# Optimization experiments

Hardware: AMD Instinct MI355X
Metric: run time of the kernel (lower is better)

The kernel has to match this reference:

```python
import jax, jax.numpy as jnp
import numpy as np

N_NODES = 15000
N_EDGES = 60000
NODE_VOCAB = 118 + 20000
EDGE_VOCAB = 4 + 50
NODE_INDIM = 64
EDGE_INDIM = 32
H = 32          # node_hidden_feats
EH = 64         # edge_hidden_feats
NUM_STEPS = 3   # num_step_message_passing
N_BOND_TYPES = 4  # edge ids < 4 are chemical bonds -> edge_func1, else knowledge relations -> edge_func2


def setup_inputs() -> dict:
    key = jax.random.key(0)
    ks = jax.random.split(key, 20)
    s = 0.05  # param scale for numerical stability
    return {
        "node_ids": jax.random.randint(ks[0], (N_NODES,), 0, NODE_VOCAB),
        "edge_ids": jax.random.randint(ks[1], (N_EDGES,), 0, EDGE_VOCAB),
        "src": jax.random.randint(ks[2], (N_EDGES,), 0, N_NODES),
        "dst": jax.random.randint(ks[3], (N_EDGES,), 0, N_NODES),
        "node_table": jax.random.normal(ks[4], (NODE_VOCAB, NODE_INDIM), jnp.float32),
        "edge_table": jax.random.normal(ks[5], (EDGE_VOCAB, EDGE_INDIM), jnp.float32),
        "proj_W": jax.random.normal(ks[6], (H, NODE_INDIM), jnp.float32) * s,
        "proj_b": jnp.zeros((H,), jnp.float32),
        "attn_w": jax.random.normal(ks[7], (2 * H,), jnp.float32) * s,
        "e1_W1": jax.random.normal(ks[8], (EH, EDGE_INDIM), jnp.float32) * s,
        "e1_b1": jnp.zeros((EH,), jnp.float32),
        "e1_W2": jax.random.normal(ks[9], (H * H, EH), jnp.float32) * s,
        "e1_b2": jnp.zeros((H * H,), jnp.float32),
        "e2_W1": jax.random.normal(ks[10], (EH, EDGE_INDIM), jnp.float32) * s,
        "e2_b1": jnp.zeros((EH,), jnp.float32),
        "e2_W2": jax.random.normal(ks[11], (H * H, EH), jnp.float32) * s,
        "e2_b2": jnp.zeros((H * H,), jnp.float32),
        "gru_Wih": jax.random.normal(ks[12], (3 * H, H), jnp.float32) * s,
        "gru_Whh": jax.random.normal(ks[13], (3 * H, H), jnp.float32) * s,
        "gru_bih": jnp.zeros((3 * H,), jnp.float32),
        "gru_bhh": jnp.zeros((3 * H,), jnp.float32),
    }


def _edge_softmax(logits, dst, num_nodes):
    # softmax over incoming edges of each destination node
    m = jax.ops.segment_max(logits, dst, num_segments=num_nodes)
    ex = jnp.exp(logits - m[dst])
    s = jax.ops.segment_sum(ex, dst, num_segments=num_nodes)
    return ex / s[dst]


def reference(node_ids, edge_ids, src, dst, node_table, edge_table, proj_W, proj_b,
              attn_w, e1_W1, e1_b1, e1_W2, e1_b2, e2_W1, e2_b1, e2_W2, e2_b2,
              gru_Wih, gru_Whh, gru_bih, gru_bhh):
    # --- embedding lookups ---
    nf = node_table[node_ids]                      # [N, node_indim]
    ef = edge_table[edge_ids]                      # [E, edge_indim]
    # --- project node feats: Linear + ReLU ---
    h = jax.nn.relu(nf @ proj_W.T + proj_b)        # [N, H]

    # --- per-edge weight matrices from the two edge MLPs (edge feats are
    # constant across message-passing steps, so compute once) ---
    def edge_mlp(W1, b1, W2, b2):
        z = jax.nn.relu(ef @ W1.T + b1)            # [E, EH]
        return (z @ W2.T + b2).reshape(-1, H, H)   # [E, H, H]

    W_e1 = edge_mlp(e1_W1, e1_b1, e1_W2, e1_b2)
    W_e2 = edge_mlp(e2_W1, e2_b1, e2_W2, e2_b2)
    is_bond = (edge_ids < N_BOND_TYPES)[:, None, None]
    W_edge = jnp.where(is_bond, W_e1, W_e2)        # [E, H, H]

    hidden = h                                     # GRU hidden state (seq of len 1 -> GRUCell)
    for _ in range(NUM_STEPS):
        # attention logits on edges: leaky_relu(attn_fc([h_src || h_dst]))
        a = jax.nn.leaky_relu(
            h[src] @ attn_w[:H] + h[dst] @ attn_w[H:])     # [E]
        alpha = _edge_softmax(a, dst, N_NODES)             # [E]
        # edge-conditioned message: (h_src @ W_e) weighted by attention
        msg = jnp.einsum('ei,eio->eo', h[src], W_edge) * alpha[:, None]  # [E, H]
        agg = jax.ops.segment_sum(msg, dst, num_segments=N_NODES)       # [N, H]
        m = jax.nn.relu(agg)
        # single GRU step (torch nn.GRU, 1 layer, seq_len 1)
        gi = m @ gru_Wih.T + gru_bih               # [N, 3H]
        gh = hidden @ gru_Whh.T + gru_bhh          # [N, 3H]
        ir, iz, inn = jnp.split(gi, 3, axis=1)
        hr, hz, hn = jnp.split(gh, 3, axis=1)
        r = jax.nn.sigmoid(ir + hr)
        z = jax.nn.sigmoid(iz + hz)
        n = jnp.tanh(inn + r * hn)
        hidden = (1.0 - z) * n + z * hidden
        h = hidden
    return h
```

## Files before the change

### kernel.cpp

```cpp
#include <hip/hip_runtime.h>
#include <math.h>

#define N_NODES   15000
#define N_EDGES   60000
#define EVOCAB    54
#define NODE_INDIM 64
#define EDGE_INDIM 32
#define H  32
#define EH 64
#define N_BOND 4

#define NPB   8
#define NBLK  (N_NODES / NPB)
#define CAPN  48

#define TASK_VOCAB (EVOCAB * 1024)
#define TASK_PROJ  (N_NODES * H)
#define TASK_EDGE_BASE (TASK_VOCAB + TASK_PROJ)
#define TA_TOTAL   (TASK_EDGE_BASE + N_EDGES)

#define WT_OFF   0
#define H0_OFF   221184
#define H1_OFF   2141184
#define W4_OFF   4061184
#define W2_OFF   4077568
#define LS0_OFF  4085760
#define BS0_OFF  4145760
#define LS1_OFF  4205760
#define BS1_OFF  4265760
#define CNT_OFF  4325760
#define EPK_OFF  4385760
#define W2T1_OFF 7265760
#define W2T2_OFF 7527904
#define PT_OFF   7790048

__global__ __launch_bounds__(256)
void pre_kernel(const float* __restrict__ e1_W2, const float* __restrict__ e2_W2,
                const float* __restrict__ proj_W,
                const float* __restrict__ gWih, const float* __restrict__ gWhh,
                float* __restrict__ W2T1, float* __restrict__ W2T2,
                float* __restrict__ PT,
                float4* __restrict__ Wpk4, float2* __restrict__ Wpk2,
                int* __restrict__ cnt)
{
    int b = blockIdx.x, tid = threadIdx.x;
    if (b < 32) {
        __shared__ float st[64][65];
        const float* in = (b < 16) ? e1_W2 : e2_W2;
        float* out      = (b < 16) ? W2T1  : W2T2;
        int f0 = (b & 15) * 64;
        #pragma unroll
        for (int it = 0; it < 16; ++it) {
            int idx = it * 256 + tid;
            int r = idx >> 6, c = idx & 63;
            st[r][c] = in[(f0 + r) * 64 + c];
        }
        __syncthreads();
        #pragma unroll
        for (int it = 0; it < 16; ++it) {
            int idx = it * 256 + tid;
            int k = idx >> 6, f = idx & 63;
            out[k * 1024 + f0 + f] = st[f][k];
        }
    } else if (b == 32) {
        __shared__ float sp2[64][33];
        #pragma unroll
        for (int it = 0; it < 8; ++it) {
            int idx = it * 256 + tid;
            int o = idx >> 6, j = idx & 63;
            sp2[j][o] = proj_W[idx];
        }
        __syncthreads();
        #pragma unroll
        for (int it = 0; it < 8; ++it) {
            int idx = it * 256 + tid;
            int j = idx >> 5, o = idx & 31;
            PT[idx] = sp2[j][o];
        }
    } else if (b <= 36) {
        int q = (b - 33) * 256 + tid;
        int j = q >> 5, o = q & 31;
        Wpk4[q] = make_float4(gWih[o * 32 + j], gWih[(32 + o) * 32 + j],
                              gWih[(64 + o) * 32 + j], gWhh[o * 32 + j]);
        Wpk2[q] = make_float2(gWhh[(32 + o) * 32 + j], gWhh[(64 + o) * 32 + j]);
    } else {
        int idx = (b - 37) * 256 + tid;
        if (idx < N_NODES) cnt[idx] = 0;
    }
}

__global__ __launch_bounds__(256)
void setup_kernel(const int* __restrict__ node_ids, const int* __restrict__ src,
                  const int* __restrict__ dst, const int* __restrict__ eid,
                  const float* __restrict__ node_table, const float* __restrict__ edge_table,
                  const float* __restrict__ PT, const float* __restrict__ proj_b,
                  const float* __restrict__ attn_w,
                  const float* __restrict__ e1_W1, const float* __restrict__ e1_b1,
                  const float* __restrict__ e1_b2,
                  const float* __restrict__ e2_W1, const float* __restrict__ e2_b1,
                  const float* __restrict__ e2_b2,
                  const float* __restrict__ W2T1, const float* __restrict__ W2T2,
                  float* __restrict__ Wt, float* __restrict__ h0,
                  float* __restrict__ ls, float* __restrict__ bs,
                  int* __restrict__ cnt, int* __restrict__ blkE)
{
    int t = blockIdx.x * 256 + threadIdx.x;
    if (t >= TA_TOTAL) return;
    if (t < TASK_VOCAB) {
        int v = t >> 10, f = t & 1023, l = t & 63;
        const float* W1  = (v < N_BOND) ? e1_W1 : e2_W1;
        const float* b1  = (v < N_BOND) ? e1_b1 : e2_b1;
        const float* b2  = (v < N_BOND) ? e1_b2 : e2_b2;
        const float* W2T = (v < N_BOND) ? W2T1  : W2T2;
        const float4* ef4 = (const float4*)(edge_table + v * EDGE_INDIM);
        const float4* w14 = (const float4*)(W1 + l * EDGE_INDIM);
        float z = b1[l];
        #pragma unroll
        for (int j = 0; j < 8; ++j) {
            float4 a = ef4[j], b = w14[j];
            z += a.x*b.x + a.y*b.y + a.z*b.z + a.w*b.w;
        }
        z = fmaxf(z, 0.f);
        float y = b2[f];
        #pragma unroll 16
        for (int k = 0; k < 64; ++k)
            y += __shfl(z, k, 64) * W2T[k * 1024 + f];
        Wt[(v << 10) + f] = y;
    } else if (t < TASK_EDGE_BASE) {
        int q = t - TASK_VOCAB;
        int n = q >> 5, o = q & 31;
        int gid = node_ids[n];
        const float* nf = node_table + (size_t)gid * NODE_INDIM;
        float nfa = nf[o], nfb = nf[32 + o];
        float acc = proj_b[o];
        #pragma unroll 8
        for (int j = 0; j < 32; ++j)
            acc += __shfl(nfa, j, 32) * PT[j * 32 + o];
        #pragma unroll 8
        for (int j = 0; j < 32; ++j)
            acc += __shfl(nfb, j, 32) * PT[(32 + j) * 32 + o];
        float hval = fmaxf(acc, 0.f);
        h0[q] = hval;
        float c1 = hval * attn_w[o], c2 = hval * attn_w[32 + o];
        #pragma unroll
        for (int k = 16; k > 0; k >>= 1) {
            c1 += __shfl_xor(c1, k, 32);
            c2 += __shfl_xor(c2, k, 32);
        }
        if (o == 0) { ls[n] = c1; bs[n] = c2; }
    } else {
        int e = t - TASK_EDGE_BASE;
        int d = dst[e];
        int pack = src[e] | (eid[e] << 14);
        int slot = atomicAdd(&cnt[d], 1);
        if (slot < CAPN) blkE[d * CAPN + slot] = pack;
    }
}

__global__ __launch_bounds__(256)
void mp_kernel(const int* __restrict__ cnt, const int* __restrict__ blkE,
               const float* __restrict__ hc, const float* __restrict__ Wt,
               const float* __restrict__ attn_w,
               const float4* __restrict__ Wpk4, const float2* __restrict__ Wpk2,
               const float* __restrict__ gbih, const float* __restrict__ gbhh,
               const float* __restrict__ lsc, const float* __restrict__ bsc,
               float* __restrict__ lsn, float* __restrict__ bsn,
               float* __restrict__ op, int last)
{
    int b = blockIdx.x, tid = threadIdx.x;
    int g = tid >> 5, o = tid & 31;
    int n = (b << 3) + g;

    int deg = cnt[n];
    if (deg > CAPN) deg = CAPN;
    int pks = blkE[n * CAPN + o];
    float hv  = hc[(n << 5) + o];
    float bdn = bsc[n];

    float sex = 0.f, acc = 0.f;
    int s = 0;
    for (; s + 1 < deg; s += 2) {
        int pk0 = __shfl(pks, s, 32);
        int pk1 = __shfl(pks, s + 1, 32);
        int sp0 = pk0 & 0x3FFF, v0 = pk0 >> 14;
        int sp1 = pk1 & 0x3FFF, v1 = pk1 >> 14;
        float a0 = lsc[sp0] + bdn; a0 = (a0 > 0.f) ? a0 : 0.01f * a0;
        float a1 = lsc[sp1] + bdn; a1 = (a1 > 0.f) ? a1 : 0.01f * a1;
        float ex0 = __expf(a0), ex1 = __expf(a1);
        float hs0 = hc[(sp0 << 5) + o];
        float hs1 = hc[(sp1 << 5) + o];
        const float* W0 = Wt + (v0 << 10) + o;
        const float* W1c = Wt + (v1 << 10) + o;
        float y0 = 0.f, y1 = 0.f;
        #pragma unroll
        for (int i = 0; i < 32; ++i) {
            y0 += __shfl(hs0, i, 32) * W0[i * 32];
            y1 += __shfl(hs1, i, 32) * W1c[i * 32];
        }
        acc += ex0 * y0 + ex1 * y1;
        sex += ex0 + ex1;
    }
    if (s < deg) {
        int pk0 = __shfl(pks, s, 32);
        int sp0 = pk0 & 0x3FFF, v0 = pk0 >> 14;
        float a0 = lsc[sp0] + bdn; a0 = (a0 > 0.f) ? a0 : 0.01f * a0;
        float ex0 = __expf(a0);
        float hs0 = hc[(sp0 << 5) + o];
        const float* W0 = Wt + (v0 << 10) + o;
        float y0 = 0.f;
        #pragma unroll
        for (int i = 0; i < 32; ++i)
            y0 += __shfl(hs0, i, 32) * W0[i * 32];
        acc += ex0 * y0;
        sex += ex0;
    }
    float m = (deg > 0) ? fmaxf(acc / sex, 0.f) : 0.f;

    float gir = 0.f, giz = 0.f, gin = 0.f, ghr = 0.f, ghz = 0.f, ghn = 0.f;
    #pragma unroll 4
    for (int j = 0; j < 32; ++j) {
        float mj = __shfl(m, j, 32);
        float hj = __shfl(hv, j, 32);
        float4 a4 = Wpk4[j * 32 + o];
        float2 b2 = Wpk2[j * 32 + o];
        gir += mj * a4.x;  giz += mj * a4.y;  gin += mj * a4.z;
        ghr += hj * a4.w;  ghz += hj * b2.x;  ghn += hj * b2.y;
    }
    float r  = 1.f / (1.f + __expf(-(gir + gbih[o]      + ghr + gbhh[o])));
    float z  = 1.f / (1.f + __expf(-(giz + gbih[32 + o] + ghz + gbhh[32 + o])));
    float nn = tanhf(gin + gbih[64 + o] + r * (ghn + gbhh[64 + o]));
    float hid = (1.f - z) * nn + z * hv;
    op[(n << 5) + o] = hid;

    if (!last) {
        float c1 = hid * attn_w[o], c2 = hid * attn_w[32 + o];
        #pragma unroll
        for (int k = 16; k > 0; k >>= 1) {
            c1 += __shfl_xor(c1, k, 32);
            c2 += __shfl_xor(c2, k, 32);
        }
        if (o == 0) { lsn[n] = c1; bsn[n] = c2; }
    }
}

extern "C" void kernel_launch(void* const* d_in, const int* in_sizes, int n_in,
                              void* d_out, int out_size, void* d_ws, size_t ws_size,
                              hipStream_t stream) {
    const int*   node_ids   = (const int*)d_in[0];
    const int*   edge_ids   = (const int*)d_in[1];
    const int*   srcp       = (const int*)d_in[2];
    const int*   dstp       = (const int*)d_in[3];
    const float* node_table = (const float*)d_in[4];
    const float* edge_table = (const float*)d_in[5];
    const float* proj_W     = (const float*)d_in[6];
    const float* proj_b     = (const float*)d_in[7];
    const float* attn_w     = (const float*)d_in[8];
    const float* e1_W1 = (const float*)d_in[9];  const float* e1_b1 = (const float*)d_in[10];
    const float* e1_W2 = (const float*)d_in[11]; const float* e1_b2 = (const float*)d_in[12];
    const float* e2_W1 = (const float*)d_in[13]; const float* e2_b1 = (const float*)d_in[14];
    const float* e2_W2 = (const float*)d_in[15]; const float* e2_b2 = (const float*)d_in[16];
    const float* gWih  = (const float*)d_in[17]; const float* gWhh  = (const float*)d_in[18];
    const float* gbih  = (const float*)d_in[19]; const float* gbhh  = (const float*)d_in[20];
    float* outp = (float*)d_out;

    char* ws = (char*)d_ws;
    float*  Wt   = (float*)(ws + WT_OFF);
    float*  h0b  = (float*)(ws + H0_OFF);
    float*  h1b  = (float*)(ws + H1_OFF);
    float4* Wpk4 = (float4*)(ws + W4_OFF);
    float2* Wpk2 = (float2*)(ws + W2_OFF);
    float*  ls0  = (float*)(ws + LS0_OFF);
    float*  bs0  = (float*)(ws + BS0_OFF);
    float*  ls1  = (float*)(ws + LS1_OFF);
    float*  bs1  = (float*)(ws + BS1_OFF);
    int*    cnt  = (int*)  (ws + CNT_OFF);
    int*    blkE = (int*)  (ws + EPK_OFF);
    float*  W2T1 = (float*)(ws + W2T1_OFF);
    float*  W2T2 = (float*)(ws + W2T2_OFF);
    float*  PT   = (float*)(ws + PT_OFF);

    pre_kernel<<<96, 256, 0, stream>>>(
        e1_W2, e2_W2, proj_W, gWih, gWhh, W2T1, W2T2, PT, Wpk4, Wpk2, cnt);

    setup_kernel<<<(TA_TOTAL + 255) / 256, 256, 0, stream>>>(
        node_ids, srcp, dstp, edge_ids, node_table, edge_table, PT, proj_b,
        attn_w, e1_W1, e1_b1, e1_b2, e2_W1, e2_b1, e2_b2, W2T1, W2T2,
        Wt, h0b, ls0, bs0, cnt, blkE);

    float* hc = h0b;  float* hn = h1b;
    float* lc = ls0;  float* bc = bs0;
    float* ln = ls1;  float* bn = bs1;
    for (int step = 0; step < 3; ++step) {
        int last = (step == 2);
        float* op = last ? outp : hn;
        mp_kernel<<<NBLK, 256, 0, stream>>>(
            cnt, blkE, hc, Wt, attn_w, Wpk4, Wpk2, gbih, gbhh,
            lc, bc, ln, bn, op, last);
        float* tf;
        tf = hc; hc = hn; hn = tf;
        tf = lc; lc = ln; ln = tf;
        tf = bc; bc = bn; bn = tf;
    }
}
```

Baseline: 219.2 us.

## Split message passing into edge-type-bucketed edge kernel and per-node aggregation kernel

Edges are now bucketed by edge vocabulary id, so each edge_kernel block runs a 32x32 matvec against one shared weight matrix using float4 loads and shuffle reductions. Each edge writes its exp-weighted message into a per-destination slot buffer, and a separate agg_kernel sums those slots and applies the GRU. The goal is better weight-cache locality and less per-lane load work than the old per-destination gather loop. The cost is a second launch per step, a large message-buffer round trip through memory, and lower caps (CAPN 24, VCAP 1280) that could silently drop edges for high-degree nodes or common edge types.

```diff
diff --git a/kernel.cpp b/kernel.cpp
--- a/kernel.cpp
+++ b/kernel.cpp
@@ -12,7 +12,10 @@
 
 #define NPB   8
 #define NBLK  (N_NODES / NPB)
-#define CAPN  48
+#define CAPN  24
+#define VCAP  1280
+#define NSLOT (EVOCAB * VCAP)
+#define EBLK  (NSLOT / 8)
 
 #define TASK_VOCAB (EVOCAB * 1024)
 #define TASK_PROJ  (N_NODES * H)
@@ -29,10 +32,15 @@
 #define LS1_OFF  4205760
 #define BS1_OFF  4265760
 #define CNT_OFF  4325760
-#define EPK_OFF  4385760
-#define W2T1_OFF 7265760
-#define W2T2_OFF 7527904
-#define PT_OFF   7790048
+#define CNTV_OFF 4385760
+#define VIDB_OFF 4386784
+#define EXB_OFF  4939744
+#define W2T1_OFF 6379744
+#define W2T2_OFF 6641888
+#define PT_OFF   6904032
+#define MSG_OFF  6912256
+
+#define ZERO_INTS ((60000 + 1024) / 4)
 
 __global__ __launch_bounds__(256)
 void pre_kernel(const float* __restrict__ e1_W2, const float* __restrict__ e2_W2,
@@ -41,7 +49,7 @@
                 float* __restrict__ W2T1, float* __restrict__ W2T2,
                 float* __restrict__ PT,
                 float4* __restrict__ Wpk4, float2* __restrict__ Wpk2,
-                int* __restrict__ cnt)
+                int* __restrict__ ctrz)
 {
     int b = blockIdx.x, tid = threadIdx.x;
     if (b < 32) {
@@ -85,7 +93,7 @@
         Wpk2[q] = make_float2(gWhh[(32 + o) * 32 + j], gWhh[(64 + o) * 32 + j]);
     } else {
         int idx = (b - 37) * 256 + tid;
-        if (idx < N_NODES) cnt[idx] = 0;
+        if (idx < ZERO_INTS) ctrz[idx] = 0;
     }
 }
 
@@ -102,7 +110,8 @@
                   const float* __restrict__ W2T1, const float* __restrict__ W2T2,
                   float* __restrict__ Wt, float* __restrict__ h0,
                   float* __restrict__ ls, float* __restrict__ bs,
-                  int* __restrict__ cnt, int* __restrict__ blkE)
+                  int* __restrict__ cnt, int* __restrict__ cntv,
+                  int2* __restrict__ vidbuf)
 {
     int t = blockIdx.x * 256 + threadIdx.x;
     if (t >= TA_TOTAL) return;
@@ -150,70 +159,76 @@
         if (o == 0) { ls[n] = c1; bs[n] = c2; }
     } else {
         int e = t - TASK_EDGE_BASE;
-        int d = dst[e];
-        int pack = src[e] | (eid[e] << 14);
-        int slot = atomicAdd(&cnt[d], 1);
-        if (slot < CAPN) blkE[d * CAPN + slot] = pack;
+        int d = dst[e], v = eid[e], sp = src[e];
+        int sv = atomicAdd(&cntv[v], 1);
+        if (sv < VCAP) {
+            int sd = atomicAdd(&cnt[d], 1);
+            int dslot = (sd < CAPN) ? (d * CAPN + sd) : -1;
+            vidbuf[v * VCAP + sv] = make_int2(sp, dslot);
+        }
     }
 }
 
 __global__ __launch_bounds__(256)
-void mp_kernel(const int* __restrict__ cnt, const int* __restrict__ blkE,
-               const float* __restrict__ hc, const float* __restrict__ Wt,
-               const float* __restrict__ attn_w,
-               const float4* __restrict__ Wpk4, const float2* __restrict__ Wpk2,
-               const float* __restrict__ gbih, const float* __restrict__ gbhh,
-               const float* __restrict__ lsc, const float* __restrict__ bsc,
-               float* __restrict__ lsn, float* __restrict__ bsn,
-               float* __restrict__ op, int last)
+void edge_kernel(const int* __restrict__ cntv, const int2* __restrict__ vidbuf,
+                 const float* __restrict__ hc, const float* __restrict__ Wt,
+                 const float* __restrict__ lsc, const float* __restrict__ bsc,
+                 float4* __restrict__ msg4, float* __restrict__ exb)
+{
+    int tid = threadIdx.x;
+    int g = tid >> 5, o = tid & 31;
+    int s = blockIdx.x * 8 + g;
+    int vid = s / VCAP;
+    int j   = s - vid * VCAP;
+    int cv = cntv[vid]; if (cv > VCAP) cv = VCAP;
+    if (j >= cv) return;
+    int2 en = vidbuf[s];
+    int sp = en.x, dslot = en.y;
+    if (dslot < 0) return;
+    int d = dslot / CAPN;
+    float a = lsc[sp] + bsc[d];
+    a = (a > 0.f) ? a : 0.01f * a;
+    float ex = __expf(a);
+    float hs = hc[(sp << 5) + o];
+    const float4* W4 = (const float4*)(Wt + (vid << 10));
+    float4 p = make_float4(0.f, 0.f, 0.f, 0.f);
+    #pragma unroll
+    for (int k = 0; k < 8; ++k) {
+        float4 w = W4[k * 32 + o];
+        float hsk = __shfl(hs, 4 * k + (o >> 3), 32);
+        p.x += hsk * w.x; p.y += hsk * w.y;
+        p.z += hsk * w.z; p.w += hsk * w.w;
+    }
+    p.x += __shfl_xor(p.x, 8, 32);  p.y += __shfl_xor(p.y, 8, 32);
+    p.z += __shfl_xor(p.z, 8, 32);  p.w += __shfl_xor(p.w, 8, 32);
+    p.x += __shfl_xor(p.x, 16, 32); p.y += __shfl_xor(p.y, 16, 32);
+    p.z += __shfl_xor(p.z, 16, 32); p.w += __shfl_xor(p.w, 16, 32);
+    if (o < 8)
+        msg4[dslot * 8 + o] = make_float4(ex * p.x, ex * p.y, ex * p.z, ex * p.w);
+    if (o == 0) exb[dslot] = ex;
+}
+
+__global__ __launch_bounds__(256)
+void agg_kernel(const int* __restrict__ cnt, const float* __restrict__ msg,
+                const float* __restrict__ exb,
+                const float* __restrict__ hc, const float* __restrict__ attn_w,
+                const float4* __restrict__ Wpk4, const float2* __restrict__ Wpk2,
+                const float* __restrict__ gbih, const float* __restrict__ gbhh,
+                float* __restrict__ lsn, float* __restrict__ bsn,
+                float* __restrict__ op, int last)
 {
     int b = blockIdx.x, tid = threadIdx.x;
     int g = tid >> 5, o = tid & 31;
     int n = (b << 3) + g;
 
-    int deg = cnt[n];
-    if (deg > CAPN) deg = CAPN;
-    int pks = blkE[n * CAPN + o];
-    float hv  = hc[(n << 5) + o];
-    float bdn = bsc[n];
-
-    float sex = 0.f, acc = 0.f;
-    int s = 0;
-    for (; s + 1 < deg; s += 2) {
-        int pk0 = __shfl(pks, s, 32);
-        int pk1 = __shfl(pks, s + 1, 32);
-        int sp0 = pk0 & 0x3FFF, v0 = pk0 >> 14;
-        int sp1 = pk1 & 0x3FFF, v1 = pk1 >> 14;
-        float a0 = lsc[sp0] + bdn; a0 = (a0 > 0.f) ? a0 : 0.01f * a0;
-        float a1 = lsc[sp1] + bdn; a1 = (a1 > 0.f) ? a1 : 0.01f * a1;
-        float ex0 = __expf(a0), ex1 = __expf(a1);
-        float hs0 = hc[(sp0 << 5) + o];
-        float hs1 = hc[(sp1 << 5) + o];
-        const float* W0 = Wt + (v0 << 10) + o;
-        const float* W1c = Wt + (v1 << 10) + o;
-        float y0 = 0.f, y1 = 0.f;
-        #pragma unroll
-        for (int i = 0; i < 32; ++i) {
-            y0 += __shfl(hs0, i, 32) * W0[i * 32];
-            y1 += __shfl(hs1, i, 32) * W1c[i * 32];
-        }
-        acc += ex0 * y0 + ex1 * y1;
-        sex += ex0 + ex1;
-    }
-    if (s < deg) {
-        int pk0 = __shfl(pks, s, 32);
-        int sp0 = pk0 & 0x3FFF, v0 = pk0 >> 14;
-        float a0 = lsc[sp0] + bdn; a0 = (a0 > 0.f) ? a0 : 0.01f * a0;
-        float ex0 = __expf(a0);
-        float hs0 = hc[(sp0 << 5) + o];
-        const float* W0 = Wt + (v0 << 10) + o;
-        float y0 = 0.f;
-        #pragma unroll
-        for (int i = 0; i < 32; ++i)
-            y0 += __shfl(hs0, i, 32) * W0[i * 32];
-        acc += ex0 * y0;
-        sex += ex0;
-    }
+    int deg = cnt[n]; if (deg > CAPN) deg = CAPN;
+    const float* mrow = msg + (size_t)n * CAPN * 32;
+    float acc = 0.f, sex = 0.f;
+    for (int j = 0; j < deg; ++j) {
+        acc += mrow[j * 32 + o];
+        sex += exb[n * CAPN + j];
+    }
+    float hv = hc[b * 256 + tid];
     float m = (deg > 0) ? fmaxf(acc / sex, 0.f) : 0.f;
 
     float gir = 0.f, giz = 0.f, gin = 0.f, ghr = 0.f, ghz = 0.f, ghn = 0.f;
@@ -274,18 +289,22 @@
     float*  ls1  = (float*)(ws + LS1_OFF);
     float*  bs1  = (float*)(ws + BS1_OFF);
     int*    cnt  = (int*)  (ws + CNT_OFF);
-    int*    blkE = (int*)  (ws + EPK_OFF);
+    int*    cntv = (int*)  (ws + CNTV_OFF);
+    int2*   vidb = (int2*) (ws + VIDB_OFF);
+    float*  exb  = (float*)(ws + EXB_OFF);
     float*  W2T1 = (float*)(ws + W2T1_OFF);
     float*  W2T2 = (float*)(ws + W2T2_OFF);
     float*  PT   = (float*)(ws + PT_OFF);
-
-    pre_kernel<<<96, 256, 0, stream>>>(
+    float*  msg  = (float*)(ws + MSG_OFF);
+    float4* msg4 = (float4*)(ws + MSG_OFF);
+
+    pre_kernel<<<97, 256, 0, stream>>>(
         e1_W2, e2_W2, proj_W, gWih, gWhh, W2T1, W2T2, PT, Wpk4, Wpk2, cnt);
 
     setup_kernel<<<(TA_TOTAL + 255) / 256, 256, 0, stream>>>(
         node_ids, srcp, dstp, edge_ids, node_table, edge_table, PT, proj_b,
         attn_w, e1_W1, e1_b1, e1_b2, e2_W1, e2_b1, e2_b2, W2T1, W2T2,
-        Wt, h0b, ls0, bs0, cnt, blkE);
+        Wt, h0b, ls0, bs0, cnt, cntv, vidb);
 
     float* hc = h0b;  float* hn = h1b;
     float* lc = ls0;  float* bc = bs0;
@@ -293,9 +312,11 @@
     for (int step = 0; step < 3; ++step) {
         int last = (step == 2);
         float* op = last ? outp : hn;
-        mp_kernel<<<NBLK, 256, 0, stream>>>(
-            cnt, blkE, hc, Wt, attn_w, Wpk4, Wpk2, gbih, gbhh,
-            lc, bc, ln, bn, op, last);
+        edge_kernel<<<EBLK, 256, 0, stream>>>(
+            cntv, vidb, hc, Wt, lc, bc, msg4, exb);
+        agg_kernel<<<NBLK, 256, 0, stream>>>(
+            cnt, msg, exb, hc, attn_w, Wpk4, Wpk2, gbih, gbhh,
+            ln, bn, op, last);
         float* tf;
         tf = hc; hc = hn; hn = tf;
         tf = lc; lc = ln; ln = tf;
```

Result: slower. 287.2 us (+31.0%).

## Bucket edges per 8-node block and aggregate messages in shared memory

Applied to the files above, without the earlier changes.

Edges are now bucketed by destination block (8 nodes) instead of per node, with the local node index packed into the edge word. The message-passing kernel stages source hidden vectors and logits in shared memory, lets all 8 warps split the block's edges evenly, computes each edge's 32x32 matvec with float4 weight loads plus shuffle reductions, and accumulates into per-node shared sums with atomics. This is meant to remove the load imbalance from differing node degrees and to coalesce weight loads, at the cost of shared-memory atomics and extra barriers. Bucket capacity is 128 edges per block, enough for the average of about 32, and the smaller counter array needs fewer zeroing blocks.

```diff
diff --git a/kernel.cpp b/kernel.cpp
--- a/kernel.cpp
+++ b/kernel.cpp
@@ -12,7 +12,7 @@
 
 #define NPB   8
 #define NBLK  (N_NODES / NPB)
-#define CAPN  48
+#define CAP   128
 
 #define TASK_VOCAB (EVOCAB * 1024)
 #define TASK_PROJ  (N_NODES * H)
@@ -29,10 +29,12 @@
 #define LS1_OFF  4205760
 #define BS1_OFF  4265760
 #define CNT_OFF  4325760
-#define EPK_OFF  4385760
-#define W2T1_OFF 7265760
-#define W2T2_OFF 7527904
-#define PT_OFF   7790048
+#define EPK_OFF  4333260
+#define W2T1_OFF 5293260
+#define W2T2_OFF 5555404
+#define PT_OFF   5817548
+
+#define ZERO_INTS 1875
 
 __global__ __launch_bounds__(256)
 void pre_kernel(const float* __restrict__ e1_W2, const float* __restrict__ e2_W2,
@@ -41,7 +43,7 @@
                 float* __restrict__ W2T1, float* __restrict__ W2T2,
                 float* __restrict__ PT,
                 float4* __restrict__ Wpk4, float2* __restrict__ Wpk2,
-                int* __restrict__ cnt)
+                int* __restrict__ ctrz)
 {
     int b = blockIdx.x, tid = threadIdx.x;
     if (b < 32) {
@@ -85,7 +87,7 @@
         Wpk2[q] = make_float2(gWhh[(32 + o) * 32 + j], gWhh[(64 + o) * 32 + j]);
     } else {
         int idx = (b - 37) * 256 + tid;
-        if (idx < N_NODES) cnt[idx] = 0;
+        if (idx < ZERO_INTS) ctrz[idx] = 0;
     }
 }
 
@@ -151,9 +153,10 @@
     } else {
         int e = t - TASK_EDGE_BASE;
         int d = dst[e];
-        int pack = src[e] | (eid[e] << 14);
-        int slot = atomicAdd(&cnt[d], 1);
-        if (slot < CAPN) blkE[d * CAPN + slot] = pack;
+        int blk = d >> 3;
+        int pos = atomicAdd(&cnt[blk], 1);
+        int pack = src[e] | (eid[e] << 14) | ((d & 7) << 20);
+        if (pos < CAP) blkE[blk * CAP + pos] = pack;
     }
 }
 
@@ -167,54 +170,66 @@
                float* __restrict__ lsn, float* __restrict__ bsn,
                float* __restrict__ op, int last)
 {
+    __shared__ float shs[CAP][32];
+    __shared__ float sagg[NPB * 32];
+    __shared__ float ssex[NPB];
+    __shared__ float slsc[CAP];
+    __shared__ int   spk[CAP];
+    __shared__ float sbs[NPB];
+
     int b = blockIdx.x, tid = threadIdx.x;
+    int cntB = cnt[b];
+    if (cntB > CAP) cntB = CAP;
+    if (tid < cntB) {
+        int pk = blkE[b * CAP + tid];
+        spk[tid]  = pk;
+        slsc[tid] = lsc[pk & 0x3FFF];
+    }
+    if (tid < NPB) { sbs[tid] = bsc[(b << 3) + tid]; ssex[tid] = 0.f; }
+    sagg[tid & 255] = 0.f;
+    __syncthreads();
+
     int g = tid >> 5, o = tid & 31;
+
+    for (int e = g; e < cntB; e += 8)
+        shs[e][o] = hc[((spk[e] & 0x3FFF) << 5) + o];
+    __syncthreads();
+
+    for (int e = g; e < cntB; e += 8) {
+        int pk = spk[e];
+        int vid = (pk >> 14) & 0x3F, dl = (pk >> 20) & 7;
+        float a = slsc[e] + sbs[dl];
+        a = (a > 0.f) ? a : 0.01f * a;
+        float ex = __expf(a);
+        float hs = shs[e][o];
+        const float4* W4 = (const float4*)(Wt + (vid << 10));
+        float4 p = make_float4(0.f, 0.f, 0.f, 0.f);
+        #pragma unroll
+        for (int k = 0; k < 8; ++k) {
+            float4 w = W4[k * 32 + o];
+            float hsk = __shfl(hs, 4 * k + (o >> 3), 32);
+            p.x += hsk * w.x; p.y += hsk * w.y;
+            p.z += hsk * w.z; p.w += hsk * w.w;
+        }
+        p.x += __shfl_xor(p.x, 8, 32);  p.y += __shfl_xor(p.y, 8, 32);
+        p.z += __shfl_xor(p.z, 8, 32);  p.w += __shfl_xor(p.w, 8, 32);
+        p.x += __shfl_xor(p.x, 16, 32); p.y += __shfl_xor(p.y, 16, 32);
+        p.z += __shfl_xor(p.z, 16, 32); p.w += __shfl_xor(p.w, 16, 32);
+        if (o < 8) {
+            float* ag = &sagg[dl * 32 + 4 * o];
+            atomicAdd(&ag[0], ex * p.x);
+            atomicAdd(&ag[1], ex * p.y);
+            atomicAdd(&ag[2], ex * p.z);
+            atomicAdd(&ag[3], ex * p.w);
+        }
+        if (o == 0) atomicAdd(&ssex[dl], ex);
+    }
+    __syncthreads();
+
     int n = (b << 3) + g;
-
-    int deg = cnt[n];
-    if (deg > CAPN) deg = CAPN;
-    int pks = blkE[n * CAPN + o];
-    float hv  = hc[(n << 5) + o];
-    float bdn = bsc[n];
-
-    float sex = 0.f, acc = 0.f;
-    int s = 0;
-    for (; s + 1 < deg; s += 2) {
-        int pk0 = __shfl(pks, s, 32);
-        int pk1 = __shfl(pks, s + 1, 32);
-        int sp0 = pk0 & 0x3FFF, v0 = pk0 >> 14;
-        int sp1 = pk1 & 0x3FFF, v1 = pk1 >> 14;
-        float a0 = lsc[sp0] + bdn; a0 = (a0 > 0.f) ? a0 : 0.01f * a0;
-        float a1 = lsc[sp1] + bdn; a1 = (a1 > 0.f) ? a1 : 0.01f * a1;
-        float ex0 = __expf(a0), ex1 = __expf(a1);
-        float hs0 = hc[(sp0 << 5) + o];
-        float hs1 = hc[(sp1 << 5) + o];
-        const float* W0 = Wt + (v0 << 10) + o;
-        const float* W1c = Wt + (v1 << 10) + o;
-        float y0 = 0.f, y1 = 0.f;
-        #pragma unroll
-        for (int i = 0; i < 32; ++i) {
-            y0 += __shfl(hs0, i, 32) * W0[i * 32];
-            y1 += __shfl(hs1, i, 32) * W1c[i * 32];
-        }
-        acc += ex0 * y0 + ex1 * y1;
-        sex += ex0 + ex1;
-    }
-    if (s < deg) {
-        int pk0 = __shfl(pks, s, 32);
-        int sp0 = pk0 & 0x3FFF, v0 = pk0 >> 14;
-        float a0 = lsc[sp0] + bdn; a0 = (a0 > 0.f) ? a0 : 0.01f * a0;
-        float ex0 = __expf(a0);
-        float hs0 = hc[(sp0 << 5) + o];
-        const float* W0 = Wt + (v0 << 10) + o;
-        float y0 = 0.f;
-        #pragma unroll
-        for (int i = 0; i < 32; ++i)
-            y0 += __shfl(hs0, i, 32) * W0[i * 32];
-        acc += ex0 * y0;
-        sex += ex0;
-    }
-    float m = (deg > 0) ? fmaxf(acc / sex, 0.f) : 0.f;
+    float sex = ssex[g];
+    float hv = hc[b * 256 + tid];
+    float m = (sex != 0.f) ? fmaxf(sagg[g * 32 + o] / sex, 0.f) : 0.f;
 
     float gir = 0.f, giz = 0.f, gin = 0.f, ghr = 0.f, ghz = 0.f, ghn = 0.f;
     #pragma unroll 4
@@ -230,7 +245,7 @@
     float z  = 1.f / (1.f + __expf(-(giz + gbih[32 + o] + ghz + gbhh[32 + o])));
     float nn = tanhf(gin + gbih[64 + o] + r * (ghn + gbhh[64 + o]));
     float hid = (1.f - z) * nn + z * hv;
-    op[(n << 5) + o] = hid;
+    op[b * 256 + tid] = hid;
 
     if (!last) {
         float c1 = hid * attn_w[o], c2 = hid * attn_w[32 + o];
@@ -279,7 +294,7 @@
     float*  W2T2 = (float*)(ws + W2T2_OFF);
     float*  PT   = (float*)(ws + PT_OFF);
 
-    pre_kernel<<<96, 256, 0, stream>>>(
+    pre_kernel<<<45, 256, 0, stream>>>(
         e1_W2, e2_W2, proj_W, gWih, gWhh, W2T1, W2T2, PT, Wpk4, Wpk2, cnt);
 
     setup_kernel<<<(TA_TOTAL + 255) / 256, 256, 0, stream>>>(
```

Measured after the change: 218.3 us. About the same (-0.4%).
